# Performance work log

Hardware: AMD Instinct MI355X
Metric: run time of the kernel (lower is better)

Reference implementation:

```python
import jax, jax.numpy as jnp
import numpy as np

SEQ_LEN = 168; PRED_LEN = 24; N_FEAT = 8; KERNEL = 25
N_QUBITS = 4; N_QLAYERS = 2; CONTEXT = 32; HIDDEN = 8; BATCH = 16384
LAG_POSITIONS = [1, 2, 3, 4, 5, 6, 23, 24, 25, 167, 168]
LAG_IDX = np.array([SEQ_LEN - l for l in LAG_POSITIONS if l <= SEQ_LEN])
N_LAGS = int(LAG_IDX.size)
PI = float(np.pi)


def _apply_1q(state, U, w):
    # apply 2x2 gate U (shared (2,2) or per-sample (B,2,2)) on wire w
    state = jnp.moveaxis(state, 1 + w, -1)
    if U.ndim == 2:
        state = jnp.einsum('ij,b...j->b...i', U, state)
    else:
        state = jnp.einsum('bij,b...j->b...i', U, state)
    return jnp.moveaxis(state, -1, 1 + w)


def _apply_cnot(state, c, t):
    ax_c, ax_t = 1 + c, 1 + t
    s0 = jax.lax.index_in_dim(state, 0, ax_c, keepdims=False)
    s1 = jax.lax.index_in_dim(state, 1, ax_c, keepdims=False)
    s1 = jnp.flip(s1, axis=ax_t - (1 if t > c else 0))
    return jnp.stack([s0, s1], axis=ax_c)


def _ry(theta):  # (B,) -> (B,2,2)
    c, s = jnp.cos(theta / 2), jnp.sin(theta / 2)
    return jnp.stack([jnp.stack([c, -s], -1), jnp.stack([s, c], -1)], -2).astype(jnp.complex64)


def _rot(w):  # w (3,): Rot(phi,theta,omega) = RZ(omega) RY(theta) RZ(phi)
    phi, theta, omega = w[0], w[1], w[2]
    c, s = jnp.cos(theta / 2), jnp.sin(theta / 2)
    ep = jnp.exp(-0.5j * (phi + omega))
    em = jnp.exp(0.5j * (phi - omega))
    return jnp.stack([jnp.stack([ep * c, -em * s]),
                      jnp.stack([jnp.conj(em) * s, jnp.conj(ep) * c])]).astype(jnp.complex64)


def _vqc(inputs, weights):
    # data re-uploading: [RY AngleEmbedding -> Rot per wire -> CNOT ring (range 1)] x N_QLAYERS
    # (StronglyEntanglingLayers is called with 1 layer per upload, so range is always 1)
    B = inputs.shape[0]
    state = jnp.zeros((B,) + (2,) * N_QUBITS, jnp.complex64)
    state = state.at[(slice(None),) + (0,) * N_QUBITS].set(1.0)
    for l in range(N_QLAYERS):
        for q in range(N_QUBITS):
            state = _apply_1q(state, _ry(inputs[:, q]), q)
        for q in range(N_QUBITS):
            state = _apply_1q(state, _rot(weights[l, q]), q)
        for q in range(N_QUBITS):
            state = _apply_cnot(state, q, (q + 1) % N_QUBITS)
    probs = state.real ** 2 + state.imag ** 2  # (B,2,2,2,2)
    zdiag = jnp.array([1.0, -1.0], jnp.float32)
    exps = []
    for q in range(N_QUBITS):
        other = tuple(a for a in range(1, N_QUBITS + 1) if a != 1 + q)
        exps.append(jnp.einsum('bq,q->b', probs.sum(other), zdiag))
    return jnp.stack(exps, axis=-1)  # (B, N_QUBITS)


def _decomp(x, decomp_w):
    # learnable moving-average decomposition (DLinear-style, per-feature softmax kernel, edge padding)
    pad = (KERNEL - 1) // 2
    w = jax.nn.softmax(decomp_w, axis=-1)  # (F,K)
    xp = jnp.pad(x, ((0, 0), (pad, KERNEL - 1 - pad), (0, 0)), mode='edge')
    xc = jnp.moveaxis(xp, 1, 2)  # (B,F,S+K-1)
    trend = jax.lax.conv_general_dilated(xc, w[:, None, :], (1,), 'VALID',
                                         feature_group_count=N_FEAT,
                                         dimension_numbers=('NCH', 'OIH', 'NCH'))
    trend = jnp.moveaxis(trend, 1, 2)  # (B,S,F)
    return x - trend, trend


def forward(x, decomp_w, trend_w, trend_b, seasonal_w, seasonal_b, h0_w, h0_b,
            ta_w, ta_b, sc_w, sc_b, crz_w, crz_b, cn_w, cn_b,
            vqc_r, vqc_u, vqc_c, expand_w, expand_b, mod_w, mod_b, fusion_alpha):
    seasonal, trend = _decomp(x, decomp_w)
    trend_out = jnp.einsum('bsf,ps->bpf', trend, trend_w) + trend_b[None, :, None]
    seasonal_base = jnp.einsum('bsf,ps->bpf', seasonal, seasonal_w) + seasonal_b[None, :, None]
    lag_vals = x[:, LAG_IDX, -1]  # (B, N_LAGS), demand is last feature
    h0 = jnp.tanh(lag_vals @ h0_w.T + h0_b)  # (B,H)
    ctx = jnp.einsum('bsf,cs->bfc', seasonal, ta_w) + ta_b  # (B,F,C)
    gru_in = jnp.tanh(ctx.reshape(x.shape[0], -1) @ sc_w.T + sc_b)  # (B,H)
    # single-step quantum GRU
    xh = jnp.concatenate([gru_in, h0], axis=1)  # (B,2H)
    rz_in = jnp.tanh(xh @ crz_w.T + crz_b) * PI  # r_in == z_in (same compress in source)
    r = jax.nn.sigmoid(_vqc(rz_in, vqc_r) @ expand_w.T + expand_b)
    z = jax.nn.sigmoid(_vqc(rz_in, vqc_u) @ expand_w.T + expand_b)
    n_in = jnp.tanh(jnp.concatenate([r * h0, gru_in], axis=1) @ cn_w.T + cn_b) * PI
    n = jnp.tanh(_vqc(n_in, vqc_c) @ expand_w.T + expand_b)
    h_new = (1 - z) * n + z * h0
    modulation = jnp.tanh(h_new @ mod_w.T + mod_b)  # (B,P)
    seasonal_out = seasonal_base * (1.0 + modulation[:, :, None])
    alpha = jax.nn.sigmoid(fusion_alpha)[0]
    return alpha * seasonal_out + (1 - alpha) * trend_out  # (B,P,F)


def setup_inputs() -> dict:
    key = jax.random.key(0)
    ks = iter(jax.random.split(key, 32))

    def lin(out_d, in_d):
        lim = 1.0 / np.sqrt(in_d)
        return (jax.random.uniform(next(ks), (out_d, in_d), jnp.float32, -lim, lim),
                jax.random.uniform(next(ks), (out_d,), jnp.float32, -lim, lim))

    trend_w, trend_b = lin(PRED_LEN, SEQ_LEN)
    seasonal_w, seasonal_b = lin(PRED_LEN, SEQ_LEN)
    h0_w, h0_b = lin(HIDDEN, N_LAGS)
    ta_w, ta_b = lin(CONTEXT, SEQ_LEN)
    sc_w, sc_b = lin(HIDDEN, N_FEAT * CONTEXT)
    crz_w, crz_b = lin(N_QUBITS, 2 * HIDDEN)
    cn_w, cn_b = lin(N_QUBITS, 2 * HIDDEN)
    expand_w, expand_b = lin(HIDDEN, N_QUBITS)
    mod_w, mod_b = lin(PRED_LEN, HIDDEN)
    return {
        'x': jax.random.normal(next(ks), (BATCH, SEQ_LEN, N_FEAT), jnp.float32),
        'decomp_w': 0.02 * jax.random.normal(next(ks), (N_FEAT, KERNEL), jnp.float32),
        'trend_w': trend_w, 'trend_b': trend_b,
        'seasonal_w': seasonal_w, 'seasonal_b': seasonal_b,
        'h0_w': h0_w, 'h0_b': h0_b,
        'ta_w': ta_w, 'ta_b': ta_b,
        'sc_w': sc_w, 'sc_b': sc_b,
        'crz_w': crz_w, 'crz_b': crz_b,
        'cn_w': cn_w, 'cn_b': cn_b,
        'vqc_r': jax.random.uniform(next(ks), (N_QLAYERS, N_QUBITS, 3), jnp.float32, 0.0, 2 * PI),
        'vqc_u': jax.random.uniform(next(ks), (N_QLAYERS, N_QUBITS, 3), jnp.float32, 0.0, 2 * PI),
        'vqc_c': jax.random.uniform(next(ks), (N_QLAYERS, N_QUBITS, 3), jnp.float32, 0.0, 2 * PI),
        'expand_w': expand_w, 'expand_b': expand_b,
        'mod_w': mod_w, 'mod_b': mod_b,
        'fusion_alpha': jnp.array([0.5], jnp.float32),
    }


def reference(x, decomp_w, trend_w, trend_b, seasonal_w, seasonal_b, h0_w, h0_b,
              ta_w, ta_b, sc_w, sc_b, crz_w, crz_b, cn_w, cn_b,
              vqc_r, vqc_u, vqc_c, expand_w, expand_b, mod_w, mod_b, fusion_alpha):
    return forward(x, decomp_w, trend_w, trend_b, seasonal_w, seasonal_b, h0_w, h0_b,
                   ta_w, ta_b, sc_w, sc_b, crz_w, crz_b, cn_w, cn_b,
                   vqc_r, vqc_u, vqc_c, expand_w, expand_b, mod_w, mod_b, fusion_alpha)
```

## Files before the change

### kernel.cpp

```cpp
#include <hip/hip_runtime.h>
#include <hip/hip_bf16.h>
#include <cmath>

#define SEQ   168
#define NF    8
#define PRED  24
#define HID   8
#define KTOT  1344
#define NSCH  6
#define PI_F  3.14159265358979323846f

#define WS_ROTC     256
#define WS_CGIN     512
#define WS_WT       1024
#define WS_Y        400000
#define WS_IMG_BYTE 524288

typedef __attribute__((ext_vector_type(8))) short bf16x8;
typedef __attribute__((ext_vector_type(4))) float f32x4;

__device__ __forceinline__ float frcp(float x)  { return __builtin_amdgcn_rcpf(x); }
__device__ __forceinline__ float ftanh(float x) {
    float xc = fminf(fmaxf(x, -15.f), 15.f);
    float e  = __expf(2.f * xc);
    return (e - 1.f) * frcp(e + 1.f);
}
__device__ __forceinline__ float sigm(float x) { return frcp(1.f + __expf(-x)); }
__device__ __forceinline__ unsigned short f2bf(float f) {
    __hip_bfloat16 h = __float2bfloat16(f);
    return __builtin_bit_cast(unsigned short, h);
}
__device__ __forceinline__ unsigned pack2(float a, float b) {
    return (unsigned)f2bf(a) | ((unsigned)f2bf(b) << 16);
}

__global__ void k_compose(const float* __restrict__ decomp_w,
                          const float* __restrict__ trend_w,
                          const float* __restrict__ seasonal_w,
                          const float* __restrict__ ta_w,
                          float* __restrict__ Wt) {
    __shared__ float dwsh[NF * 25];
    int t = threadIdx.x;
    if (t < NF) {
        const float* row = decomp_w + t * 25;
        float m = row[0];
        for (int k = 1; k < 25; ++k) m = fmaxf(m, row[k]);
        float e[25]; float sum = 0.f;
        for (int k = 0; k < 25; ++k) { e[k] = expf(row[k] - m); sum += e[k]; }
        float inv = 1.f / sum;
        for (int k = 0; k < 25; ++k) dwsh[t * 25 + k] = e[k] * inv;
    }
    __syncthreads();
    int n = blockIdx.x * 256 + t;
    if (n >= SEQ * 640) return;
    int sx  = n / 640;
    int col = n % 640;
    int j = col >> 3;
    int f = col & 7;
    const float* dwf = dwsh + f * 25;
    const float* wsel;
    int isTrend = 0;
    if (j < 24)      { wsel = trend_w    + j        * SEQ; isTrend = 1; }
    else if (j < 48) { wsel = seasonal_w + (j - 24) * SEQ; }
    else             { wsel = ta_w       + (j - 48) * SEQ; }
    float acc = 0.f;
    if (sx == 0) {
        for (int s = 0; s <= 12; ++s) {
            float cw = 0.f;
            for (int k = 0; k <= 12 - s; ++k) cw += dwf[k];
            acc = fmaf(cw, wsel[s], acc);
        }
    } else if (sx == 167) {
        for (int s = 155; s < 168; ++s) {
            float cw = 0.f;
            for (int k = 179 - s; k < 25; ++k) cw += dwf[k];
            acc = fmaf(cw, wsel[s], acc);
        }
    } else {
        int lo = sx - 12; if (lo < 0) lo = 0;
        int hi = sx + 12; if (hi > 167) hi = 167;
        for (int s = lo; s <= hi; ++s) acc = fmaf(dwf[sx - s + 12], wsel[s], acc);
    }
    Wt[sx * 640 + col] = isTrend ? acc : (wsel[sx] - acc);
}

__global__ void k_img(const float* __restrict__ Wt, const float* __restrict__ sc_w,
                      const float* __restrict__ h0_w,
                      const float* __restrict__ vr, const float* __restrict__ vu,
                      const float* __restrict__ vc,
                      const float* __restrict__ sc_b, const float* __restrict__ ta_b,
                      float* __restrict__ rotc, float* __restrict__ cgin,
                      unsigned char* __restrict__ imgb) {
    int idx = blockIdx.x * 256 + threadIdx.x;
    if (idx < 12288) {
        int lane = idx & 63;
        int rest = idx >> 6;
        int ks = rest % 6;
        int fc = rest / 6;
        int cf = fc & 3, f = fc >> 2;
        int lr = lane & 15, lg = lane >> 4;
        unsigned short vals[8];
        #pragma unroll
        for (int e = 0; e < 8; ++e) {
            int k = ks * 32 + lg * 8 + e;
            float val = 0.f;
            if (k < SEQ) {
                if (cf < 3) {
                    int c = cf * 16 + lr;
                    int ts = (c >= 24);
                    int p  = ts ? (c - 24) : c;
                    val = Wt[k * 640 + ts * 192 + p * 8 + f];
                } else if (lr < 8) {
                    float a = 0.f;
                    for (int cc = 0; cc < 32; ++cc)
                        a = fmaf(sc_w[lr * 256 + f * 32 + cc], Wt[k * 640 + 384 + cc * 8 + f], a);
                    val = a;
                } else if (f == 7) {
                    const int LIDX[11] = {167,166,165,164,163,162,145,144,143,1,0};
                    #pragma unroll
                    for (int i = 0; i < 11; ++i)
                        if (k == LIDX[i]) val = h0_w[(lr - 8) * 11 + i];
                }
            }
            vals[e] = f2bf(val);
        }
        uint4 o;
        o.x = (unsigned)vals[0] | ((unsigned)vals[1] << 16);
        o.y = (unsigned)vals[2] | ((unsigned)vals[3] << 16);
        o.z = (unsigned)vals[4] | ((unsigned)vals[5] << 16);
        o.w = (unsigned)vals[6] | ((unsigned)vals[7] << 16);
        *(uint4*)(imgb + (size_t)rest * 1024 + lane * 16) = o;
    } else if (blockIdx.x == 48) {
        int t = threadIdx.x;
        if (t >= 64 && t < 88) {
            int n = t - 64;
            int v = n / 8, rest = n % 8;
            const float* w = (v == 0 ? vr : (v == 1 ? vu : vc)) + rest * 3;
            float phi = w[0], th = w[1], om = w[2];
            float c = cosf(0.5f * th), s = sinf(0.5f * th);
            float ap = -0.5f * (phi + om);
            float am =  0.5f * (phi - om);
            float* o = rotc + n * 4;
            o[0] = cosf(ap) * c;
            o[1] = sinf(ap) * c;
            o[2] = cosf(am) * s;
            o[3] = sinf(am) * s;
        } else if (t >= 96 && t < 104) {
            int h = t - 96;
            float a = sc_b[h];
            for (int cc = 0; cc < 32; ++cc) {
                float s = 0.f;
                for (int f = 0; f < 8; ++f) s += sc_w[h * 256 + f * 32 + cc];
                a = fmaf(ta_b[cc], s, a);
            }
            cgin[h] = a;
        }
    }
}

__global__ __launch_bounds__(512, 2)
void k_gemm(const float* __restrict__ x, const unsigned char* __restrict__ img,
            float* __restrict__ y, int Btot)
{
    __shared__ unsigned char lds[49152];
    float* ghpart = (float*)(lds + 32768);

    const int t    = threadIdx.x;
    const int b0   = blockIdx.x * 32;
    const int w    = t >> 6, lane = t & 63, lr = lane & 15, lg = lane >> 4;

    const int arow  = t >> 4;
    const int spair = t & 15;
    int gr = b0 + arow; if (gr >= Btot) gr = Btot - 1;
    const float* xrow = x + (size_t)gr * KTOT;
    const unsigned char* ib = img + (size_t)(w * 24) * 1024 + (size_t)lane * 16;

    float4 raA[4], raB[4];
    #pragma unroll
    for (int u = 0; u < 4; ++u) raA[u] = *(const float4*)&xrow[spair * 16 + u * 4];
    #pragma unroll
    for (int u = 0; u < 4; ++u) raB[u] = *(const float4*)&xrow[256 + spair * 16 + u * 4];
    bf16x8 BrA[4], BrB[4];
    #pragma unroll
    for (int cf = 0; cf < 4; ++cf) BrA[cf] = *(const bf16x8*)&ib[(cf * 6 + 0) * 1024];
    #pragma unroll
    for (int cf = 0; cf < 4; ++cf) BrB[cf] = *(const bf16x8*)&ib[(cf * 6 + 1) * 1024];

    f32x4 acc[3][2], accg[2];
    #pragma unroll
    for (int cf = 0; cf < 3; ++cf) {
        acc[cf][0] = (f32x4){0.f, 0.f, 0.f, 0.f};
        acc[cf][1] = (f32x4){0.f, 0.f, 0.f, 0.f};
    }
    accg[0] = (f32x4){0.f, 0.f, 0.f, 0.f};
    accg[1] = (f32x4){0.f, 0.f, 0.f, 0.f};

    const int wb   = (arow * 64 + spair * 4) ^ ((arow & 7) << 4);
    const int ar0  = (lr * 64 + lg * 16) ^ ((lr & 7) << 4);
    const int ar1  = ((lr + 16) * 64 + lg * 16) ^ ((lr & 7) << 4);

    #pragma unroll
    for (int kc = 0; kc < NSCH; ++kc) {
        const int bufo = (kc & 1) * 16384;
        {
            const float* rf = (kc & 1) ? (const float*)raB : (const float*)raA;
            #pragma unroll
            for (int f = 0; f < 8; ++f)
                *(unsigned*)&lds[bufo + f * 2048 + wb] = pack2(rf[f], rf[8 + f]);
        }
        if (kc + 2 < NSCH) {
            int off = (kc + 2) * 256 + spair * 16;
            if (off > KTOT - 16) off = KTOT - 16;
            if (kc & 1) {
                #pragma unroll
                for (int u = 0; u < 4; ++u) raB[u] = *(const float4*)&xrow[off + u * 4];
            } else {
                #pragma unroll
                for (int u = 0; u < 4; ++u) raA[u] = *(const float4*)&xrow[off + u * 4];
            }
        }
        __syncthreads();
        {
            bf16x8 a0 = *(const bf16x8*)&lds[bufo + w * 2048 + ar0];
            bf16x8 a1 = *(const bf16x8*)&lds[bufo + w * 2048 + ar1];
            if (kc & 1) {
                #pragma unroll
                for (int cf = 0; cf < 3; ++cf) {
                    acc[cf][0] = __builtin_amdgcn_mfma_f32_16x16x32_bf16(a0, BrB[cf], acc[cf][0], 0, 0, 0);
                    acc[cf][1] = __builtin_amdgcn_mfma_f32_16x16x32_bf16(a1, BrB[cf], acc[cf][1], 0, 0, 0);
                }
                accg[0] = __builtin_amdgcn_mfma_f32_16x16x32_bf16(a0, BrB[3], accg[0], 0, 0, 0);
                accg[1] = __builtin_amdgcn_mfma_f32_16x16x32_bf16(a1, BrB[3], accg[1], 0, 0, 0);
            } else {
                #pragma unroll
                for (int cf = 0; cf < 3; ++cf) {
                    acc[cf][0] = __builtin_amdgcn_mfma_f32_16x16x32_bf16(a0, BrA[cf], acc[cf][0], 0, 0, 0);
                    acc[cf][1] = __builtin_amdgcn_mfma_f32_16x16x32_bf16(a1, BrA[cf], acc[cf][1], 0, 0, 0);
                }
                accg[0] = __builtin_amdgcn_mfma_f32_16x16x32_bf16(a0, BrA[3], accg[0], 0, 0, 0);
                accg[1] = __builtin_amdgcn_mfma_f32_16x16x32_bf16(a1, BrA[3], accg[1], 0, 0, 0);
            }
        }
        if (kc + 2 < NSCH) {
            if (kc & 1) {
                #pragma unroll
                for (int cf = 0; cf < 4; ++cf) BrB[cf] = *(const bf16x8*)&ib[(cf * 6 + kc + 2) * 1024];
            } else {
                #pragma unroll
                for (int cf = 0; cf < 4; ++cf) BrA[cf] = *(const bf16x8*)&ib[(cf * 6 + kc + 2) * 1024];
            }
        }
    }

    #pragma unroll
    for (int cf = 0; cf < 3; ++cf) {
        int c = cf * 16 + lr;
        int base = (c < 24) ? (w * 24 + c) : (192 + w * 24 + (c - 24));
        #pragma unroll
        for (int mf = 0; mf < 2; ++mf) {
            #pragma unroll
            for (int reg = 0; reg < 4; ++reg) {
                int R = b0 + mf * 16 + lg * 4 + reg;
                if (R < Btot) y[(size_t)R * 400 + base] = (mf ? acc[cf][1][reg] : acc[cf][0][reg]);
            }
        }
    }

    #pragma unroll
    for (int mf = 0; mf < 2; ++mf)
        #pragma unroll
        for (int reg = 0; reg < 4; ++reg)
            ghpart[(w * 32 + mf * 16 + lg * 4 + reg) * 16 + lr] = accg[mf][reg];
    __syncthreads();
    {
        int row = t >> 4, col = t & 15;
        float s = 0.f;
        #pragma unroll
        for (int f = 0; f < 8; ++f) s += ghpart[f * 512 + row * 16 + col];
        int R = b0 + row;
        if (R < Btot) y[(size_t)R * 400 + 384 + col] = s;
    }
}

__device__ __forceinline__ float shflg(float v, int grp, int idx) {
    return __shfl(v, grp + idx, 64);
}

__device__ void vqc_run(const float cq[4], const float sq[4],
                        const float* __restrict__ rc,
                        int l, int grp, float exps[4]) {
    float re = (l == 0) ? 1.f : 0.f;
    float im = 0.f;
    #pragma unroll
    for (int layer = 0; layer < 2; ++layer) {
        #pragma unroll
        for (int q = 0; q < 4; ++q) {
            int m = 1 << (3 - q);
            float pre = shflg(re, grp, l ^ m);
            float pim = shflg(im, grp, l ^ m);
            float sg = (l & m) ? sq[q] : -sq[q];
            re = cq[q] * re + sg * pre;
            im = cq[q] * im + sg * pim;
        }
        #pragma unroll
        for (int q = 0; q < 4; ++q) {
            int m = 1 << (3 - q);
            const float* g = rc + (layer * 4 + q) * 4;
            float A = g[0], B = g[1], C = g[2], D = g[3];
            float pre = shflg(re, grp, l ^ m);
            float pim = shflg(im, grp, l ^ m);
            float car, cai, cpr, cpi;
            if (l & m) { car = A; cai = -B; cpr =  C; cpi = -D; }
            else       { car = A; cai =  B; cpr = -C; cpi = -D; }
            float nre = car * re - cai * im + cpr * pre - cpi * pim;
            float nim = car * im + cai * re + cpr * pim + cpi * pre;
            re = nre; im = nim;
        }
        #pragma unroll
        for (int q = 0; q < 4; ++q) {
            int mc = 1 << (3 - q);
            int mt = 1 << (3 - ((q + 1) & 3));
            float pre = shflg(re, grp, l ^ mt);
            float pim = shflg(im, grp, l ^ mt);
            if (l & mc) { re = pre; im = pim; }
        }
    }
    float prob = re * re + im * im;
    float v0 = (l & 8) ? -prob : prob;
    float v1 = (l & 4) ? -prob : prob;
    float v2 = (l & 2) ? -prob : prob;
    float v3 = (l & 1) ? -prob : prob;
    #pragma unroll
    for (int m = 1; m < 16; m <<= 1) {
        v0 += __shfl_xor(v0, m, 64);
        v1 += __shfl_xor(v1, m, 64);
        v2 += __shfl_xor(v2, m, 64);
        v3 += __shfl_xor(v3, m, 64);
    }
    exps[0] = v0; exps[1] = v1; exps[2] = v2; exps[3] = v3;
}

__global__ __launch_bounds__(256)
void k_post(const float* __restrict__ y, const float* __restrict__ rotc,
            const float* __restrict__ cgin, const float* __restrict__ h0_b,
            const float* __restrict__ crz_w, const float* __restrict__ crz_b,
            const float* __restrict__ cn_w, const float* __restrict__ cn_b,
            const float* __restrict__ expand_w, const float* __restrict__ expand_b,
            const float* __restrict__ mod_w, const float* __restrict__ mod_b,
            const float* __restrict__ trend_b, const float* __restrict__ seasonal_b,
            const float* __restrict__ fusion_alpha,
            float* __restrict__ out, int Btot)
{
    __shared__ float yb[16 * 400];
    __shared__ float modt[16 * 25];
    const int t  = threadIdx.x;
    const int b0 = blockIdx.x * 16;

    #pragma unroll
    for (int i = 0; i < 7; ++i) {
        int idx = t + i * 256;
        if (idx < 1600) {
            int r = idx / 100, cu = idx % 100;
            int R = b0 + r; if (R >= Btot) R = Btot - 1;
            *(float4*)&yb[r * 400 + cu * 4] = *(const float4*)&y[(size_t)R * 400 + cu * 4];
        }
    }
    __syncthreads();

    {
        const int rl  = t >> 4;
        const int l   = t & 15;
        const int lane = t & 63;
        const int grp = lane & 48;
        float gin[HID], h0v[HID];
        #pragma unroll
        for (int h = 0; h < HID; ++h) {
            gin[h] = ftanh(yb[rl * 400 + 384 + h] + cgin[h]);
            h0v[h] = ftanh(yb[rl * 400 + 392 + h] + h0_b[h]);
        }
        float rz[4];
        #pragma unroll
        for (int q = 0; q < 4; ++q) {
            float a = crz_b[q];
            #pragma unroll
            for (int k = 0; k < 8; ++k) a = fmaf(gin[k], crz_w[q * 16 + k], a);
            #pragma unroll
            for (int k = 0; k < 8; ++k) a = fmaf(h0v[k], crz_w[q * 16 + 8 + k], a);
            rz[q] = ftanh(a) * PI_F;
        }
        float cq[4], sq[4];
        #pragma unroll
        for (int q = 0; q < 4; ++q) { cq[q] = __cosf(0.5f * rz[q]); sq[q] = __sinf(0.5f * rz[q]); }

        float er[4], ez[4];
        vqc_run(cq, sq, rotc + 0 * 32, l, grp, er);
        vqc_run(cq, sq, rotc + 1 * 32, l, grp, ez);

        float rr[HID], zz[HID];
        #pragma unroll
        for (int h = 0; h < HID; ++h) {
            float a = expand_b[h], b = expand_b[h];
            #pragma unroll
            for (int q = 0; q < 4; ++q) {
                a = fmaf(er[q], expand_w[h * 4 + q], a);
                b = fmaf(ez[q], expand_w[h * 4 + q], b);
            }
            rr[h] = sigm(a);
            zz[h] = sigm(b);
        }
        float ni[4];
        #pragma unroll
        for (int q = 0; q < 4; ++q) {
            float a = cn_b[q];
            #pragma unroll
            for (int k = 0; k < 8; ++k) a = fmaf(rr[k] * h0v[k], cn_w[q * 16 + k], a);
            #pragma unroll
            for (int k = 0; k < 8; ++k) a = fmaf(gin[k], cn_w[q * 16 + 8 + k], a);
            ni[q] = ftanh(a) * PI_F;
        }
        #pragma unroll
        for (int q = 0; q < 4; ++q) { cq[q] = __cosf(0.5f * ni[q]); sq[q] = __sinf(0.5f * ni[q]); }
        float en[4];
        vqc_run(cq, sq, rotc + 2 * 32, l, grp, en);

        float hn[HID];
        #pragma unroll
        for (int h = 0; h < HID; ++h) {
            float a = expand_b[h];
            #pragma unroll
            for (int q = 0; q < 4; ++q) a = fmaf(en[q], expand_w[h * 4 + q], a);
            float nn = ftanh(a);
            hn[h] = (1.f - zz[h]) * nn + zz[h] * h0v[h];
        }
        int pp = l;
        float a = mod_b[pp];
        #pragma unroll
        for (int h = 0; h < HID; ++h) a = fmaf(hn[h], mod_w[pp * 8 + h], a);
        modt[rl * 25 + pp] = ftanh(a);
        if (l < 8) {
            pp = l + 16;
            a = mod_b[pp];
            #pragma unroll
            for (int h = 0; h < HID; ++h) a = fmaf(hn[h], mod_w[pp * 8 + h], a);
            modt[rl * 25 + pp] = ftanh(a);
        }
    }
    __syncthreads();

    const float alpha = sigm(fusion_alpha[0]);
    #pragma unroll
    for (int i = 0; i < 12; ++i) {
        int idx = t + i * 256;
        int r = idx / 192, o = idx % 192;
        int R = b0 + r;
        if (R < Btot) {
            int p = o >> 3, f = o & 7;
            float T = yb[r * 400 + f * 24 + p];
            float S = yb[r * 400 + 192 + f * 24 + p];
            float md = modt[r * 25 + p];
            out[(size_t)R * 192 + o] = alpha * ((S + seasonal_b[p]) * (1.f + md))
                                     + (1.f - alpha) * (T + trend_b[p]);
        }
    }
}

extern "C" void kernel_launch(void* const* d_in, const int* in_sizes, int n_in,
                              void* d_out, int out_size, void* d_ws, size_t ws_size,
                              hipStream_t stream) {
    const float* x          = (const float*)d_in[0];
    const float* decomp_w   = (const float*)d_in[1];
    const float* trend_w    = (const float*)d_in[2];
    const float* trend_b    = (const float*)d_in[3];
    const float* seasonal_w = (const float*)d_in[4];
    const float* seasonal_b = (const float*)d_in[5];
    const float* h0_w       = (const float*)d_in[6];
    const float* h0_b       = (const float*)d_in[7];
    const float* ta_w       = (const float*)d_in[8];
    const float* ta_b       = (const float*)d_in[9];
    const float* sc_w       = (const float*)d_in[10];
    const float* sc_b       = (const float*)d_in[11];
    const float* crz_w      = (const float*)d_in[12];
    const float* crz_b      = (const float*)d_in[13];
    const float* cn_w       = (const float*)d_in[14];
    const float* cn_b       = (const float*)d_in[15];
    const float* vqc_r      = (const float*)d_in[16];
    const float* vqc_u      = (const float*)d_in[17];
    const float* vqc_c      = (const float*)d_in[18];
    const float* expand_w   = (const float*)d_in[19];
    const float* expand_b   = (const float*)d_in[20];
    const float* mod_w      = (const float*)d_in[21];
    const float* mod_b      = (const float*)d_in[22];
    const float* fus_a      = (const float*)d_in[23];
    float* out = (float*)d_out;

    float* ws   = (float*)d_ws;
    float* rotc = ws + WS_ROTC;
    float* cgin = ws + WS_CGIN;
    float* Wt   = ws + WS_WT;
    float* y    = ws + WS_Y;
    unsigned char* img = (unsigned char*)d_ws + WS_IMG_BYTE;

    const int Btot = in_sizes[0] / (SEQ * NF);

    k_compose<<<(SEQ * 640 + 255) / 256, 256, 0, stream>>>(decomp_w, trend_w, seasonal_w, ta_w, Wt);
    k_img<<<49, 256, 0, stream>>>(Wt, sc_w, h0_w, vqc_r, vqc_u, vqc_c, sc_b, ta_b,
                                  rotc, cgin, img);

    k_gemm<<<(Btot + 31) / 32, 512, 0, stream>>>(x, img, y, Btot);

    k_post<<<(Btot + 15) / 16, 256, 0, stream>>>(y, rotc, cgin, h0_b,
                                                 crz_w, crz_b, cn_w, cn_b,
                                                 expand_w, expand_b, mod_w, mod_b,
                                                 trend_b, seasonal_b, fus_a, out, Btot);
}
```

Before: 60.63 us.

## Split GEMM reduction dimension across two grid halves and sum partials in post

The GEMM kernel now launches a second grid dimension. Each half handles three of the six K-chunks and writes its partial result to its own buffer, and the post kernel adds the two partial buffers when loading. LDS is halved, the launch bound goes from 2 to 3 blocks per CU, and the double-buffered register prefetch of B fragments is replaced by a single load per chunk. The aim is more blocks and higher occupancy, at the cost of an extra full-size intermediate write and read, plus less latency hiding on B loads.

Measured after the change: 65.49 us. 8.0% more time.

```diff
diff --git a/kernel.cpp b/kernel.cpp
--- a/kernel.cpp
+++ b/kernel.cpp
@@ -7,13 +7,13 @@
 #define PRED  24
 #define HID   8
 #define KTOT  1344
-#define NSCH  6
 #define PI_F  3.14159265358979323846f
 
 #define WS_ROTC     256
 #define WS_CGIN     512
 #define WS_WT       1024
-#define WS_Y        400000
+#define WS_Y0       1000000
+#define WS_Y1       8000000
 #define WS_IMG_BYTE 524288
 
 typedef __attribute__((ext_vector_type(8))) short bf16x8;
@@ -158,15 +158,17 @@
     }
 }
 
-__global__ __launch_bounds__(512, 2)
+__global__ __launch_bounds__(512, 3)
 void k_gemm(const float* __restrict__ x, const unsigned char* __restrict__ img,
-            float* __restrict__ y, int Btot)
+            float* __restrict__ y0, float* __restrict__ y1, int Btot)
 {
-    __shared__ unsigned char lds[49152];
-    float* ghpart = (float*)(lds + 32768);
+    __shared__ unsigned char lds[32768];
+    float* ghpart = (float*)(lds + 16384);
 
     const int t    = threadIdx.x;
     const int b0   = blockIdx.x * 32;
+    const int kh   = blockIdx.y;
+    float* y = kh ? y1 : y0;
     const int w    = t >> 6, lane = t & 63, lr = lane & 15, lg = lane >> 4;
 
     const int arow  = t >> 4;
@@ -175,16 +177,12 @@
     const float* xrow = x + (size_t)gr * KTOT;
     const unsigned char* ib = img + (size_t)(w * 24) * 1024 + (size_t)lane * 16;
 
-    float4 raA[4], raB[4];
-    #pragma unroll
-    for (int u = 0; u < 4; ++u) raA[u] = *(const float4*)&xrow[spair * 16 + u * 4];
-    #pragma unroll
-    for (int u = 0; u < 4; ++u) raB[u] = *(const float4*)&xrow[256 + spair * 16 + u * 4];
-    bf16x8 BrA[4], BrB[4];
-    #pragma unroll
-    for (int cf = 0; cf < 4; ++cf) BrA[cf] = *(const bf16x8*)&ib[(cf * 6 + 0) * 1024];
-    #pragma unroll
-    for (int cf = 0; cf < 4; ++cf) BrB[cf] = *(const bf16x8*)&ib[(cf * 6 + 1) * 1024];
+    float4 ra[4];
+    {
+        int off = kh * 768 + spair * 16;
+        #pragma unroll
+        for (int u = 0; u < 4; ++u) ra[u] = *(const float4*)&xrow[off + u * 4];
+    }
 
     f32x4 acc[3][2], accg[2];
     #pragma unroll
@@ -200,55 +198,35 @@
     const int ar1  = ((lr + 16) * 64 + lg * 16) ^ ((lr & 7) << 4);
 
     #pragma unroll
-    for (int kc = 0; kc < NSCH; ++kc) {
+    for (int kc = 0; kc < 3; ++kc) {
+        const int ac   = kh * 3 + kc;
         const int bufo = (kc & 1) * 16384;
         {
-            const float* rf = (kc & 1) ? (const float*)raB : (const float*)raA;
+            const float* rf = (const float*)ra;
             #pragma unroll
             for (int f = 0; f < 8; ++f)
                 *(unsigned*)&lds[bufo + f * 2048 + wb] = pack2(rf[f], rf[8 + f]);
         }
-        if (kc + 2 < NSCH) {
-            int off = (kc + 2) * 256 + spair * 16;
+        if (kc + 1 < 3) {
+            int off = (ac + 1) * 256 + spair * 16;
             if (off > KTOT - 16) off = KTOT - 16;
-            if (kc & 1) {
-                #pragma unroll
-                for (int u = 0; u < 4; ++u) raB[u] = *(const float4*)&xrow[off + u * 4];
-            } else {
-                #pragma unroll
-                for (int u = 0; u < 4; ++u) raA[u] = *(const float4*)&xrow[off + u * 4];
-            }
-        }
+            #pragma unroll
+            for (int u = 0; u < 4; ++u) ra[u] = *(const float4*)&xrow[off + u * 4];
+        }
+        bf16x8 Br[4];
+        #pragma unroll
+        for (int cf = 0; cf < 4; ++cf) Br[cf] = *(const bf16x8*)&ib[(cf * 6 + ac) * 1024];
         __syncthreads();
         {
             bf16x8 a0 = *(const bf16x8*)&lds[bufo + w * 2048 + ar0];
             bf16x8 a1 = *(const bf16x8*)&lds[bufo + w * 2048 + ar1];
-            if (kc & 1) {
-                #pragma unroll
-                for (int cf = 0; cf < 3; ++cf) {
-                    acc[cf][0] = __builtin_amdgcn_mfma_f32_16x16x32_bf16(a0, BrB[cf], acc[cf][0], 0, 0, 0);
-                    acc[cf][1] = __builtin_amdgcn_mfma_f32_16x16x32_bf16(a1, BrB[cf], acc[cf][1], 0, 0, 0);
-                }
-                accg[0] = __builtin_amdgcn_mfma_f32_16x16x32_bf16(a0, BrB[3], accg[0], 0, 0, 0);
-                accg[1] = __builtin_amdgcn_mfma_f32_16x16x32_bf16(a1, BrB[3], accg[1], 0, 0, 0);
-            } else {
-                #pragma unroll
-                for (int cf = 0; cf < 3; ++cf) {
-                    acc[cf][0] = __builtin_amdgcn_mfma_f32_16x16x32_bf16(a0, BrA[cf], acc[cf][0], 0, 0, 0);
-                    acc[cf][1] = __builtin_amdgcn_mfma_f32_16x16x32_bf16(a1, BrA[cf], acc[cf][1], 0, 0, 0);
-                }
-                accg[0] = __builtin_amdgcn_mfma_f32_16x16x32_bf16(a0, BrA[3], accg[0], 0, 0, 0);
-                accg[1] = __builtin_amdgcn_mfma_f32_16x16x32_bf16(a1, BrA[3], accg[1], 0, 0, 0);
+            #pragma unroll
+            for (int cf = 0; cf < 3; ++cf) {
+                acc[cf][0] = __builtin_amdgcn_mfma_f32_16x16x32_bf16(a0, Br[cf], acc[cf][0], 0, 0, 0);
+                acc[cf][1] = __builtin_amdgcn_mfma_f32_16x16x32_bf16(a1, Br[cf], acc[cf][1], 0, 0, 0);
             }
-        }
-        if (kc + 2 < NSCH) {
-            if (kc & 1) {
-                #pragma unroll
-                for (int cf = 0; cf < 4; ++cf) BrB[cf] = *(const bf16x8*)&ib[(cf * 6 + kc + 2) * 1024];
-            } else {
-                #pragma unroll
-                for (int cf = 0; cf < 4; ++cf) BrA[cf] = *(const bf16x8*)&ib[(cf * 6 + kc + 2) * 1024];
-            }
+            accg[0] = __builtin_amdgcn_mfma_f32_16x16x32_bf16(a0, Br[3], accg[0], 0, 0, 0);
+            accg[1] = __builtin_amdgcn_mfma_f32_16x16x32_bf16(a1, Br[3], accg[1], 0, 0, 0);
         }
     }
 
@@ -341,7 +319,8 @@
 }
 
 __global__ __launch_bounds__(256)
-void k_post(const float* __restrict__ y, const float* __restrict__ rotc,
+void k_post(const float* __restrict__ y0, const float* __restrict__ y1,
+            const float* __restrict__ rotc,
             const float* __restrict__ cgin, const float* __restrict__ h0_b,
             const float* __restrict__ crz_w, const float* __restrict__ crz_b,
             const float* __restrict__ cn_w, const float* __restrict__ cn_b,
@@ -362,7 +341,10 @@
         if (idx < 1600) {
             int r = idx / 100, cu = idx % 100;
             int R = b0 + r; if (R >= Btot) R = Btot - 1;
-            *(float4*)&yb[r * 400 + cu * 4] = *(const float4*)&y[(size_t)R * 400 + cu * 4];
+            float4 a = *(const float4*)&y0[(size_t)R * 400 + cu * 4];
+            float4 b = *(const float4*)&y1[(size_t)R * 400 + cu * 4];
+            float4 s; s.x = a.x + b.x; s.y = a.y + b.y; s.z = a.z + b.z; s.w = a.w + b.w;
+            *(float4*)&yb[r * 400 + cu * 4] = s;
         }
     }
     __syncthreads();
@@ -497,7 +479,8 @@
     float* rotc = ws + WS_ROTC;
     float* cgin = ws + WS_CGIN;
     float* Wt   = ws + WS_WT;
-    float* y    = ws + WS_Y;
+    float* y0   = ws + WS_Y0;
+    float* y1   = ws + WS_Y1;
     unsigned char* img = (unsigned char*)d_ws + WS_IMG_BYTE;
 
     const int Btot = in_sizes[0] / (SEQ * NF);
@@ -506,9 +489,10 @@
     k_img<<<49, 256, 0, stream>>>(Wt, sc_w, h0_w, vqc_r, vqc_u, vqc_c, sc_b, ta_b,
                                   rotc, cgin, img);
 
-    k_gemm<<<(Btot + 31) / 32, 512, 0, stream>>>(x, img, y, Btot);
-
-    k_post<<<(Btot + 15) / 16, 256, 0, stream>>>(y, rotc, cgin, h0_b,
+    dim3 ggrid((Btot + 31) / 32, 2);
+    k_gemm<<<ggrid, 512, 0, stream>>>(x, img, y0, y1, Btot);
+
+    k_post<<<(Btot + 15) / 16, 256, 0, stream>>>(y0, y1, rotc, cgin, h0_b,
                                                  crz_w, crz_b, cn_w, cn_b,
                                                  expand_w, expand_b, mod_w, mod_b,
                                                  trend_b, seasonal_b, fus_a, out, Btot);
```
